# Optimization experiments

Measured on AMD Instinct MI355X. Metric: run time of the kernel, lower is better.

## Reference

```python
import jax, jax.numpy as jnp
import numpy as np

NUM_CLASSES = 81
THRESHOLD = 0.5
NEG_POS = 3
VAR = (0.1, 0.2)


def _point_form(p):
    # center form (cx,cy,w,h) -> corner form (xmin,ymin,xmax,ymax)
    return jnp.concatenate([p[:, :2] - p[:, 2:] / 2, p[:, :2] + p[:, 2:] / 2], axis=1)


def _iou(a, b):
    # a: [T,4] corner-form truths, b: [P,4] corner-form priors -> [T,P]
    lt = jnp.maximum(a[:, None, :2], b[None, :, :2])
    rb = jnp.minimum(a[:, None, 2:], b[None, :, 2:])
    wh = jnp.clip(rb - lt, 0.0)
    inter = wh[..., 0] * wh[..., 1]
    area_a = (a[:, 2] - a[:, 0]) * (a[:, 3] - a[:, 1])
    area_b = (b[:, 2] - b[:, 0]) * (b[:, 3] - b[:, 1])
    return inter / (area_a[:, None] + area_b[None, :] - inter)


def _match_one(truths, labels, priors, priors_pf):
    # SSD match(): bipartite-force best prior per truth, then threshold the rest.
    T = truths.shape[0]
    ov = _iou(truths, priors_pf)                       # [T, P]
    best_prior_idx = jnp.argmax(ov, axis=1)            # [T]
    best_truth_ov = jnp.max(ov, axis=0)                # [P]
    best_truth_idx = jnp.argmax(ov, axis=0)            # [P]
    best_truth_ov = best_truth_ov.at[best_prior_idx].set(2.0)
    best_truth_idx = best_truth_idx.at[best_prior_idx].set(jnp.arange(T))
    matched = truths[best_truth_idx]                   # [P,4]
    conf = labels[best_truth_idx] + 1
    conf = jnp.where(best_truth_ov < THRESHOLD, 0, conf)
    # encode(matched, priors, variances)
    g_cxcy = ((matched[:, :2] + matched[:, 2:]) / 2 - priors[:, :2]) / (VAR[0] * priors[:, 2:])
    g_wh = jnp.log((matched[:, 2:] - matched[:, :2]) / priors[:, 2:]) / VAR[1]
    return jnp.concatenate([g_cxcy, g_wh], axis=1), conf


def setup_inputs() -> dict:
    key = jax.random.key(0)
    k1, k2, k3, k4, k5, k6 = jax.random.split(key, 6)
    B, P, T, C = 32, 24564, 50, NUM_CLASSES
    loc_data = jax.random.normal(k1, (B, P, 4), jnp.float32)
    conf_data = jax.random.normal(k2, (B, P, C), jnp.float32)
    cxy = jax.random.uniform(k3, (P, 2), jnp.float32, 0.05, 0.95)
    pwh = jax.random.uniform(k4, (P, 2), jnp.float32, 0.05, 0.3)
    priors = jnp.concatenate([cxy, pwh], axis=1)       # center form, all w/h > 0
    bmin = jax.random.uniform(k5, (B, T, 2), jnp.float32, 0.0, 0.65)
    bwh = jax.random.uniform(jax.random.fold_in(k5, 1), (B, T, 2), jnp.float32, 0.05, 0.3)
    boxes = jnp.concatenate([bmin, bmin + bwh], axis=2)  # valid corner-form boxes
    labels = jax.random.randint(k6, (B, T), 0, C - 1, jnp.int32)  # 0..79 -> conf 1..80
    return {"loc_data": loc_data, "conf_data": conf_data, "priors": priors,
            "boxes": boxes, "labels": labels}


def reference(loc_data, conf_data, priors, boxes, labels):
    B, P, C = conf_data.shape
    priors_pf = _point_form(priors)
    loc_t, conf_t = jax.vmap(lambda t, l: _match_one(t, l, priors, priors_pf))(boxes, labels)
    pos = conf_t > 0                                   # [B,P]
    # localization: smooth-L1 (beta=1) summed over positive priors
    d = loc_data - loc_t
    ad = jnp.abs(d)
    sl1 = jnp.where(ad < 1.0, 0.5 * d * d, ad - 0.5).sum(-1)
    loss_l = jnp.sum(jnp.where(pos, sl1, 0.0))
    # per-prior cross entropy
    logp = jax.nn.log_softmax(conf_data, axis=-1)
    ce = -jnp.take_along_axis(logp, conf_t[..., None], axis=-1)[..., 0]  # [B,P]
    # hard negative mining via the double-argsort rank trick
    mine = jnp.where(pos, 0.0, ce)
    loss_idx = jnp.argsort(-mine, axis=1)
    idx_rank = jnp.argsort(loss_idx, axis=1)
    num_pos = pos.sum(axis=1, keepdims=True)
    num_neg = jnp.clip(NEG_POS * num_pos, None, P - 1)
    neg = idx_rank < num_neg
    loss_c = jnp.sum(jnp.where(pos | neg, ce, 0.0))
    N = num_pos.sum().astype(loc_data.dtype)
    return loss_l / N, loss_c / N
```

## Files before the change

kernel.cpp:

```cpp
#include <hip/hip_runtime.h>
#include <cstdint>
#include <cstddef>

constexpr int B = 32;
constexpr int P = 24564;
constexpr int T = 50;
constexpr int C = 81;

__global__ __launch_bounds__(512) void k_match_truth(
    const float* __restrict__ priors, const float* __restrict__ boxes,
    unsigned long long* __restrict__ gkey,
    int* __restrict__ num_pos, float* __restrict__ accum)
{
  if (blockIdx.x == 0 && blockIdx.y == 0) {
    if (threadIdx.x < B) num_pos[threadIdx.x] = 0;
    else if (threadIdx.x < B + 2) accum[threadIdx.x - B] = 0.0f;
  }
  const int b = blockIdx.y;
  const int t0 = blockIdx.x * 2;
  float x0[2], y0[2], x1[2], y1[2], aa[2];
#pragma unroll
  for (int j = 0; j < 2; ++j) {
    const float4 bx = reinterpret_cast<const float4*>(boxes)[b * T + t0 + j];
    x0[j] = bx.x; y0[j] = bx.y; x1[j] = bx.z; y1[j] = bx.w;
    aa[j] = (x1[j] - x0[j]) * (y1[j] - y0[j]);
  }
  unsigned long long key0 = 0ull, key1 = 0ull;
  for (int p = threadIdx.x; p < P; p += 512) {
    const float4 pr = reinterpret_cast<const float4*>(priors)[p];
    const float bx0 = pr.x - pr.z * 0.5f, by0 = pr.y - pr.w * 0.5f;
    const float bx1 = pr.x + pr.z * 0.5f, by1 = pr.y + pr.w * 0.5f;
    const float area_b = (bx1 - bx0) * (by1 - by0);
    const unsigned pk = 0xFFFFFFFFu - (unsigned)p;
    {
      const float lx = fmaxf(x0[0], bx0), ly = fmaxf(y0[0], by0);
      const float rx = fminf(x1[0], bx1), ry = fminf(y1[0], by1);
      const float w = fmaxf(rx - lx, 0.f), h = fmaxf(ry - ly, 0.f);
      const float inter = w * h;
      const float iou = __fdividef(inter, aa[0] + area_b - inter);
      const unsigned long long kk =
          ((unsigned long long)__float_as_uint(iou) << 32) | pk;
      key0 = kk > key0 ? kk : key0;
    }
    {
      const float lx = fmaxf(x0[1], bx0), ly = fmaxf(y0[1], by0);
      const float rx = fminf(x1[1], bx1), ry = fminf(y1[1], by1);
      const float w = fmaxf(rx - lx, 0.f), h = fmaxf(ry - ly, 0.f);
      const float inter = w * h;
      const float iou = __fdividef(inter, aa[1] + area_b - inter);
      const unsigned long long kk =
          ((unsigned long long)__float_as_uint(iou) << 32) | pk;
      key1 = kk > key1 ? kk : key1;
    }
  }
  const int lane = threadIdx.x & 63, wv = threadIdx.x >> 6;
  __shared__ unsigned long long sred[2][8];
#pragma unroll
  for (int o = 32; o > 0; o >>= 1) {
    const unsigned long long o0 = __shfl_xor(key0, o);
    const unsigned long long o1 = __shfl_xor(key1, o);
    key0 = o0 > key0 ? o0 : key0;
    key1 = o1 > key1 ? o1 : key1;
  }
  if (lane == 0) { sred[0][wv] = key0; sred[1][wv] = key1; }
  __syncthreads();
  if (threadIdx.x < 2) {
    unsigned long long m = sred[threadIdx.x][0];
#pragma unroll
    for (int w2 = 1; w2 < 8; ++w2)
      m = sred[threadIdx.x][w2] > m ? sred[threadIdx.x][w2] : m;
    gkey[b * T + t0 + threadIdx.x] = m;
  }
}

__global__ __launch_bounds__(256) void k_ce_fused(
    const float* __restrict__ conf_data, const float* __restrict__ loc_data,
    const float* __restrict__ priors, const float* __restrict__ boxes,
    const int* __restrict__ labels, const unsigned long long* __restrict__ gkey,
    float* __restrict__ mine, int* __restrict__ num_pos, float* __restrict__ accum)
{
  const int b = blockIdx.y;
  const int row0 = blockIdx.x * 256;
  const int nrows = min(256, P - row0);
  const int tid = threadIdx.x;

  __shared__ int sconf[256];
  __shared__ float sbuf[64 * 81];
  __shared__ float sredf[4];
  __shared__ float sredc[4];
  __shared__ int sredi[4];

  const float* __restrict__ bx = boxes + (size_t)b * T * 4;
  const unsigned* __restrict__ gk32 =
      reinterpret_cast<const unsigned*>(gkey + (size_t)b * T);

  float locs = 0.0f;
  int isp = 0;
  int myconf = 0;
  const int p = row0 + tid;
  if (p < P) {
    const float4 pr = reinterpret_cast<const float4*>(priors)[p];
    const float bx0 = pr.x - pr.z * 0.5f, by0 = pr.y - pr.w * 0.5f;
    const float bx1 = pr.x + pr.z * 0.5f, by1 = pr.y + pr.w * 0.5f;
    const float area_b = (bx1 - bx0) * (by1 - by0);
    float best = -1.0f; int bt = 0; int ovt = -1;
    for (int t = 0; t < T; ++t) {
      const float4 tb = reinterpret_cast<const float4*>(bx)[t];
      const float ta = (tb.z - tb.x) * (tb.w - tb.y);
      const float lx = fmaxf(tb.x, bx0), ly = fmaxf(tb.y, by0);
      const float rx = fminf(tb.z, bx1), ry = fminf(tb.w, by1);
      const float w = fmaxf(rx - lx, 0.f), h = fmaxf(ry - ly, 0.f);
      const float inter = w * h;
      const float iou = __fdividef(inter, ta + area_b - inter);
      if (iou > best) { best = iou; bt = t; }
      const int op = (int)(0xFFFFFFFFu - gk32[2 * t]);
      if (op == p) ovt = t;
    }
    float ov; int t;
    if (ovt >= 0) { ov = 2.0f; t = ovt; } else { ov = best; t = bt; }
    myconf = (ov < 0.5f) ? 0 : (labels[b * T + t] + 1);
    if (myconf > 0) {
      isp = 1;
      const float4 tb = reinterpret_cast<const float4*>(bx)[t];
      const float gx = __fdividef((tb.x + tb.z) * 0.5f - pr.x, 0.1f * pr.z);
      const float gy = __fdividef((tb.y + tb.w) * 0.5f - pr.y, 0.1f * pr.w);
      const float gw = __logf(__fdividef(tb.z - tb.x, pr.z)) * 5.0f;
      const float gh = __logf(__fdividef(tb.w - tb.y, pr.w)) * 5.0f;
      const float4 ld = reinterpret_cast<const float4*>(loc_data)[(size_t)b * P + p];
      float d, ad;
      d = ld.x - gx; ad = fabsf(d); locs += (ad < 1.f) ? 0.5f * d * d : ad - 0.5f;
      d = ld.y - gy; ad = fabsf(d); locs += (ad < 1.f) ? 0.5f * d * d : ad - 0.5f;
      d = ld.z - gw; ad = fabsf(d); locs += (ad < 1.f) ? 0.5f * d * d : ad - 0.5f;
      d = ld.w - gh; ad = fabsf(d); locs += (ad < 1.f) ? 0.5f * d * d : ad - 0.5f;
    }
  }
  sconf[tid] = myconf;

  const float* __restrict__ batch = conf_data + (size_t)b * P * C;
  float acc = 0.0f;
  for (int c = 0; c < 4; ++c) {
    const int r0 = c * 64;
    const int nr = min(64, nrows - r0);
    __syncthreads();
    const int nf4 = (nr * 81) >> 2;
    const float4* gsrc =
        reinterpret_cast<const float4*>(batch + (size_t)(row0 + r0) * C);
    for (int i = tid; i < nf4; i += 256)
      reinterpret_cast<float4*>(sbuf)[i] = gsrc[i];
    __syncthreads();
    const int r = tid >> 2, q = tid & 3;
    if (r < nr) {
      const int j0 = (q == 0) ? 0 : (1 + 20 * q);
      const int nj = (q == 0) ? 21 : 20;
      const float* src = sbuf + r * 81;
      float s = 0.0f;
      for (int j = 0; j < nj; ++j) s += __expf(src[j0 + j]);
      const int tgt = sconf[r0 + r];
      float xt = (tgt >= j0 && tgt < j0 + nj) ? src[tgt] : 0.0f;
      s += __shfl_xor(s, 1); xt += __shfl_xor(xt, 1);
      s += __shfl_xor(s, 2); xt += __shfl_xor(xt, 2);
      if (q == 0) {
        const float ce = __logf(s) - xt;
        const float mv = (tgt > 0) ? 0.0f : ce;
        mine[(size_t)b * P + row0 + r0 + r] = mv;
        acc += ce - mv;
      }
    }
  }

#pragma unroll
  for (int o = 32; o > 0; o >>= 1) {
    locs += __shfl_xor(locs, o);
    acc  += __shfl_xor(acc, o);
    isp  += __shfl_xor(isp, o);
  }
  const int lane = tid & 63, wv = tid >> 6;
  if (lane == 0) { sredf[wv] = locs; sredc[wv] = acc; sredi[wv] = isp; }
  __syncthreads();
  if (tid == 0) {
    const float L = sredf[0] + sredf[1] + sredf[2] + sredf[3];
    const float A = sredc[0] + sredc[1] + sredc[2] + sredc[3];
    const int   I = sredi[0] + sredi[1] + sredi[2] + sredi[3];
    if (L != 0.f) atomicAdd(&accum[0], L);
    if (A != 0.f) atomicAdd(&accum[1], A);
    if (I) atomicAdd(&num_pos[b], I);
  }
}

__global__ __launch_bounds__(1024) void k_select(
    const float* __restrict__ mine, const int* __restrict__ num_pos,
    float* __restrict__ accum)
{
  const int b = blockIdx.x;
  int k = 3 * num_pos[b];
  if (k > P - 1) k = P - 1;
  if (k <= 0) return;
  const float* __restrict__ vm = mine + (size_t)b * P;
  __shared__ unsigned hist[4096];
  __shared__ unsigned s_prefix, s_rem;
  __shared__ float sredf[16];
  if (threadIdx.x == 0) { s_prefix = 0u; s_rem = (unsigned)k; }

  const int shifts[3] = {20, 8, 0};
  const int nbs[3]    = {4096, 4096, 256};
  const unsigned hms[3] = {0u, 0xFFF00000u, 0xFFFFFF00u};

  for (int pass = 0; pass < 3; ++pass) {
    const int shift = shifts[pass];
    const int nb = nbs[pass];
    const unsigned hm = hms[pass];
    for (int i = threadIdx.x; i < nb; i += 1024) hist[i] = 0u;
    __syncthreads();
    const unsigned pfx = s_prefix;
    for (int i = threadIdx.x; i < P; i += 1024) {
      const unsigned bits = __float_as_uint(vm[i]);
      if ((bits & hm) == pfx) atomicAdd(&hist[(bits >> shift) & (nb - 1)], 1u);
    }
    __syncthreads();
    if (threadIdx.x < 64) {
      const int lane = threadIdx.x;
      const int gsz = nb >> 6;
      unsigned tot = 0u;
      for (int m = 0; m < gsz; ++m) tot += hist[lane * gsz + m];
      unsigned t = tot;
#pragma unroll
      for (int o = 1; o < 64; o <<= 1) {
        const unsigned v = __shfl_down(t, o);
        t += (lane + o < 64) ? v : 0u;
      }
      const unsigned rem0 = s_rem;
      const unsigned above = t - tot;
      const bool selg = (t >= rem0) && (above < rem0);
      const unsigned long long bal = __ballot(selg);
      const int g = (int)(__ffsll((unsigned long long)bal) - 1);
      const unsigned rem2 = rem0 - __shfl(above, g);
      unsigned hb = (lane < gsz) ? hist[g * gsz + lane] : 0u;
      unsigned t2 = hb;
#pragma unroll
      for (int o = 1; o < 64; o <<= 1) {
        const unsigned v = __shfl_down(t2, o);
        t2 += (lane + o < 64) ? v : 0u;
      }
      if ((lane < gsz) && (t2 >= rem2) && (t2 - hb < rem2)) {
        s_prefix = pfx | ((unsigned)(g * gsz + lane) << shift);
        s_rem = rem2 - (t2 - hb);
      }
    }
    __syncthreads();
  }
  const unsigned cut = s_prefix;
  const unsigned remc = s_rem;
  float acc = 0.0f;
  for (int i = threadIdx.x; i < P; i += 1024) {
    const float v = vm[i];
    acc += (__float_as_uint(v) > cut) ? v : 0.0f;
  }
#pragma unroll
  for (int o = 32; o > 0; o >>= 1) acc += __shfl_xor(acc, o);
  const int lane = threadIdx.x & 63, wv = threadIdx.x >> 6;
  if (lane == 0) sredf[wv] = acc;
  __syncthreads();
  if (threadIdx.x == 0) {
    float tot = 0.f;
#pragma unroll
    for (int w2 = 0; w2 < 16; ++w2) tot += sredf[w2];
    tot += (float)remc * __uint_as_float(cut);
    atomicAdd(&accum[1], tot);
  }
}

__global__ void k_final(const int* __restrict__ num_pos,
                        const float* __restrict__ accum, float* __restrict__ out)
{
  if (threadIdx.x == 0 && blockIdx.x == 0) {
    int N = 0;
#pragma unroll
    for (int b = 0; b < B; ++b) N += num_pos[b];
    const float fN = (float)N;
    out[0] = accum[0] / fN;
    out[1] = accum[1] / fN;
  }
}

extern "C" void kernel_launch(void* const* d_in, const int* in_sizes, int n_in,
                              void* d_out, int out_size, void* d_ws, size_t ws_size,
                              hipStream_t stream)
{
  (void)in_sizes; (void)n_in; (void)out_size; (void)ws_size;
  const float* loc_data  = (const float*)d_in[0];
  const float* conf_data = (const float*)d_in[1];
  const float* priors    = (const float*)d_in[2];
  const float* boxes     = (const float*)d_in[3];
  const int*   labels    = (const int*)d_in[4];
  float* out = (float*)d_out;

  char* ws = (char*)d_ws;
  const size_t BP = (size_t)B * P;
  float* mine = (float*)ws;
  unsigned long long* gkey = (unsigned long long*)(ws + BP * 4);
  int* num_pos = (int*)(ws + BP * 4 + (size_t)(B * T * 8));
  float* accum = (float*)(ws + BP * 4 + (size_t)(B * T * 8) + 128);

  k_match_truth<<<dim3(T / 2, B), 512, 0, stream>>>(priors, boxes, gkey,
                                                    num_pos, accum);
  k_ce_fused<<<dim3((P + 255) / 256, B), 256, 0, stream>>>(
      conf_data, loc_data, priors, boxes, labels, gkey, mine, num_pos, accum);
  k_select<<<B, 1024, 0, stream>>>(mine, num_pos, accum);
  k_final<<<1, 64, 0, stream>>>(num_pos, accum, out);
}
```

Measured before the change: 456.6 us.

## Double-buffer conf tiles via async global-to-LDS loads and cache truth boxes in LDS

The fused CE kernel now stages conf_data rows into a double-buffered LDS tile using the global_load_lds builtin. The load for the next 64-row chunk is issued before the current chunk is processed, and the first chunk is issued before the IoU matching loop, so memory traffic overlaps compute. Truth boxes are cached in LDS. The per-prior search for a forced-match override, formerly a scan of the global keys, is replaced by a per-block scatter into a local table. The cost is much more LDS per block, which can lower occupancy, and the code now relies on barriers to order the asynchronous LDS writes before they are read.

```diff
diff --git a/kernel.cpp b/kernel.cpp
--- a/kernel.cpp
+++ b/kernel.cpp
@@ -6,6 +6,11 @@
 constexpr int P = 24564;
 constexpr int T = 50;
 constexpr int C = 81;
+
+typedef __attribute__((address_space(3))) void lds_void;
+typedef const __attribute__((address_space(1))) void gbl_void;
+#define GLOAD_LDS16(gp, lp) \
+  __builtin_amdgcn_global_load_lds((gbl_void*)(gp), (lds_void*)(lp), 16, 0, 0)
 
 __global__ __launch_bounds__(512) void k_match_truth(
     const float* __restrict__ priors, const float* __restrict__ boxes,
@@ -81,18 +86,51 @@
 {
   const int b = blockIdx.y;
   const int row0 = blockIdx.x * 256;
-  const int nrows = min(256, P - row0);
+  const int nrows = (P - row0 < 256) ? (P - row0) : 256;
   const int tid = threadIdx.x;
 
+  __shared__ float sbuf[2 * 5376];
+  __shared__ float4 tbb[T];
+  __shared__ int ovr_local[256];
   __shared__ int sconf[256];
-  __shared__ float sbuf[64 * 81];
-  __shared__ float sredf[4];
-  __shared__ float sredc[4];
+  __shared__ float sredf[4], sredc[4];
   __shared__ int sredi[4];
 
-  const float* __restrict__ bx = boxes + (size_t)b * T * 4;
   const unsigned* __restrict__ gk32 =
       reinterpret_cast<const unsigned*>(gkey + (size_t)b * T);
+
+  ovr_local[tid] = -1;
+  if (tid < T) tbb[tid] = reinterpret_cast<const float4*>(boxes)[b * T + tid];
+  __syncthreads();
+  if (tid < T) {
+    const int op = (int)(0xFFFFFFFFu - gk32[2 * tid]);
+    const int loc = op - row0;
+    if (loc >= 0 && loc < 256) atomicMax(&ovr_local[loc], tid);
+  }
+  __syncthreads();
+
+  const float4* __restrict__ cf4 = reinterpret_cast<const float4*>(conf_data);
+  const size_t TOTF4 = ((size_t)B * P * C) >> 2;
+  const size_t bbase = ((size_t)b * P * C + (size_t)row0 * C) >> 2;
+
+  auto stage = [&](int c, int sel) {
+    const size_t cb = bbase + (size_t)c * 1296;
+    float4* lb = reinterpret_cast<float4*>(sbuf) + sel * 1344;
+#pragma unroll
+    for (int it = 0; it < 5; ++it) {
+      size_t gi = cb + it * 256 + tid;
+      gi = (gi < TOTF4) ? gi : (TOTF4 - 1);
+      GLOAD_LDS16(cf4 + gi, lb + it * 256 + (tid & ~63));
+    }
+    if (tid < 64) {
+      const int rel = (1280 + tid < 1296) ? (1280 + tid) : 1295;
+      size_t gi = cb + rel;
+      gi = (gi < TOTF4) ? gi : (TOTF4 - 1);
+      GLOAD_LDS16(cf4 + gi, lb + 1280);
+    }
+  };
+
+  stage(0, 0);
 
   float locs = 0.0f;
   int isp = 0;
@@ -103,9 +141,9 @@
     const float bx0 = pr.x - pr.z * 0.5f, by0 = pr.y - pr.w * 0.5f;
     const float bx1 = pr.x + pr.z * 0.5f, by1 = pr.y + pr.w * 0.5f;
     const float area_b = (bx1 - bx0) * (by1 - by0);
-    float best = -1.0f; int bt = 0; int ovt = -1;
+    float best = -1.0f; int bt = 0;
     for (int t = 0; t < T; ++t) {
-      const float4 tb = reinterpret_cast<const float4*>(bx)[t];
+      const float4 tb = tbb[t];
       const float ta = (tb.z - tb.x) * (tb.w - tb.y);
       const float lx = fmaxf(tb.x, bx0), ly = fmaxf(tb.y, by0);
       const float rx = fminf(tb.z, bx1), ry = fminf(tb.w, by1);
@@ -113,15 +151,14 @@
       const float inter = w * h;
       const float iou = __fdividef(inter, ta + area_b - inter);
       if (iou > best) { best = iou; bt = t; }
-      const int op = (int)(0xFFFFFFFFu - gk32[2 * t]);
-      if (op == p) ovt = t;
-    }
+    }
+    const int ovt = ovr_local[tid];
     float ov; int t;
     if (ovt >= 0) { ov = 2.0f; t = ovt; } else { ov = best; t = bt; }
     myconf = (ov < 0.5f) ? 0 : (labels[b * T + t] + 1);
     if (myconf > 0) {
       isp = 1;
-      const float4 tb = reinterpret_cast<const float4*>(bx)[t];
+      const float4 tb = tbb[t];
       const float gx = __fdividef((tb.x + tb.z) * 0.5f - pr.x, 0.1f * pr.z);
       const float gy = __fdividef((tb.y + tb.w) * 0.5f - pr.y, 0.1f * pr.w);
       const float gw = __logf(__fdividef(tb.z - tb.x, pr.z)) * 5.0f;
@@ -135,37 +172,34 @@
     }
   }
   sconf[tid] = myconf;
-
-  const float* __restrict__ batch = conf_data + (size_t)b * P * C;
+  __syncthreads();
+
+  const size_t mbase = (size_t)b * P + row0;
   float acc = 0.0f;
   for (int c = 0; c < 4; ++c) {
-    const int r0 = c * 64;
-    const int nr = min(64, nrows - r0);
-    __syncthreads();
-    const int nf4 = (nr * 81) >> 2;
-    const float4* gsrc =
-        reinterpret_cast<const float4*>(batch + (size_t)(row0 + r0) * C);
-    for (int i = tid; i < nf4; i += 256)
-      reinterpret_cast<float4*>(sbuf)[i] = gsrc[i];
-    __syncthreads();
+    if (c < 3) stage(c + 1, (c + 1) & 1);
+    const int nr0 = nrows - c * 64;
+    const int nr = (nr0 < 64) ? nr0 : 64;
+    const float* src0 = sbuf + (c & 1) * 5376;
     const int r = tid >> 2, q = tid & 3;
     if (r < nr) {
       const int j0 = (q == 0) ? 0 : (1 + 20 * q);
       const int nj = (q == 0) ? 21 : 20;
-      const float* src = sbuf + r * 81;
+      const float* src = src0 + r * 81;
       float s = 0.0f;
       for (int j = 0; j < nj; ++j) s += __expf(src[j0 + j]);
-      const int tgt = sconf[r0 + r];
+      const int tgt = sconf[c * 64 + r];
       float xt = (tgt >= j0 && tgt < j0 + nj) ? src[tgt] : 0.0f;
       s += __shfl_xor(s, 1); xt += __shfl_xor(xt, 1);
       s += __shfl_xor(s, 2); xt += __shfl_xor(xt, 2);
       if (q == 0) {
         const float ce = __logf(s) - xt;
         const float mv = (tgt > 0) ? 0.0f : ce;
-        mine[(size_t)b * P + row0 + r0 + r] = mv;
+        mine[mbase + c * 64 + r] = mv;
         acc += ce - mv;
       }
     }
+    __syncthreads();
   }
 
 #pragma unroll
```

Result: faster. 438.6 us (-3.9%).
